# Kernel tuning notes

Measured on AMD Instinct MI355X. Metric: run time of the kernel, lower is better.

## Reference

```python
import jax, jax.numpy as jnp
import numpy as np

TWO_PI = 6.283185  # constant used verbatim in the original module


def setup_inputs() -> dict:
    key = jax.random.key(0)
    ks = jax.random.split(key, 12)
    N, input_size, light_freq, H = 8388608, 11, 16, 16
    d_in = input_size - 2 + 2 * light_freq  # 41
    x = jax.random.uniform(ks[0], (N, input_size), dtype=jnp.float32)
    B_light = jax.random.normal(ks[1], (2, light_freq), dtype=jnp.float32)
    W1 = jax.random.normal(ks[2], (d_in, H), dtype=jnp.float32) * (1.0 / np.sqrt(d_in))
    b1 = jax.random.normal(ks[3], (H,), dtype=jnp.float32) * 0.01
    W2 = jax.random.normal(ks[4], (H, H), dtype=jnp.float32) * 0.25
    b2 = jax.random.normal(ks[5], (H,), dtype=jnp.float32) * 0.01
    W3 = jax.random.normal(ks[6], (H, H), dtype=jnp.float32) * 0.25
    b3 = jax.random.normal(ks[7], (H,), dtype=jnp.float32) * 0.01
    W4 = jax.random.normal(ks[8], (H, H), dtype=jnp.float32) * 0.25
    b4 = jax.random.normal(ks[9], (H,), dtype=jnp.float32) * 0.01
    W5 = jax.random.normal(ks[10], (H, 1), dtype=jnp.float32) * 0.25
    b5 = jax.random.normal(ks[11], (1,), dtype=jnp.float32) * 0.01
    return {"x": x, "B_light": B_light, "W1": W1, "b1": b1, "W2": W2, "b2": b2,
            "W3": W3, "b3": b3, "W4": W4, "b4": b4, "W5": W5, "b5": b5}


def reference(x, B_light, W1, b1, W2, b2, W3, b3, W4, b4, W5, b5):
    # Fourier-feature encoding of the last two input dims (light direction)
    x_light = TWO_PI * (x[:, -2:] @ B_light)                      # [N, F]
    feats = jnp.concatenate([x[:, :-2], jnp.cos(x_light), jnp.sin(x_light)], axis=-1)  # [N, 41]
    # Tiny 5-layer MLP with ELU activations
    h = jax.nn.elu(feats @ W1 + b1)
    h = jax.nn.elu(h @ W2 + b2)
    h = jax.nn.elu(h @ W3 + b3)
    h = jax.nn.elu(h @ W4 + b4)
    out = h @ W5 + b5                                             # [N, 1]
    return out
```

## Files before the change

### kernel.cpp

```cpp
#include <hip/hip_runtime.h>

typedef __fp16   cvt16x2 __attribute__((ext_vector_type(2)));
typedef _Float16 h2      __attribute__((ext_vector_type(2)));
typedef _Float16 half4_t __attribute__((ext_vector_type(4)));
typedef unsigned uint2v  __attribute__((ext_vector_type(2)));
typedef float    f32x4   __attribute__((ext_vector_type(4)));

#define CH 8

#if !__has_builtin(__builtin_elementwise_exp2)
extern "C" __device__ _Float16 __ocml_exp2_f16(_Float16);
#endif

__device__ __forceinline__ unsigned pk(float a, float b) {
    cvt16x2 h = __builtin_amdgcn_cvt_pkrtz(a, b);
    return __builtin_bit_cast(unsigned, h);
}
__device__ __forceinline__ half4_t mkfrag(unsigned lo, unsigned hi) {
    uint2v u; u[0] = lo; u[1] = hi;
    return __builtin_bit_cast(half4_t, u);
}

__device__ __forceinline__ unsigned elu_pk(float a, float b) {
    h2 v = __builtin_bit_cast(h2, __builtin_amdgcn_cvt_pkrtz(a, b));
    const h2 z  = {(_Float16)0.f, (_Float16)0.f};
    const h2 lg = {(_Float16)1.44269504f, (_Float16)1.44269504f};
    const h2 m1 = {(_Float16)-1.f, (_Float16)-1.f};
    h2 t = __builtin_elementwise_min(v, z) * lg;
#if __has_builtin(__builtin_elementwise_exp2)
    h2 ev = __builtin_elementwise_exp2(t);
#else
    h2 ev; ev[0] = __ocml_exp2_f16(t[0]); ev[1] = __ocml_exp2_f16(t[1]);
#endif
    h2 r = __builtin_elementwise_max(v, ev + m1);
    return __builtin_bit_cast(unsigned, r);
}

__device__ __forceinline__ float hdot2(unsigned a, unsigned b, float c) {
#if __has_builtin(__builtin_amdgcn_fdot2)
    return __builtin_amdgcn_fdot2(__builtin_bit_cast(cvt16x2, a),
                                  __builtin_bit_cast(cvt16x2, b), c, false);
#else
    h2 av = __builtin_bit_cast(h2, a), bv = __builtin_bit_cast(h2, b);
    return fmaf((float)av[1], (float)bv[1], fmaf((float)av[0], (float)bv[0], c));
#endif
}

__global__ __launch_bounds__(128, 4) void pixenc_mfma6(
    const float* __restrict__ x,
    const float* __restrict__ Bl,
    const float* __restrict__ W1, const float* __restrict__ b1,
    const float* __restrict__ W2, const float* __restrict__ b2,
    const float* __restrict__ W3, const float* __restrict__ b3,
    const float* __restrict__ W4, const float* __restrict__ b4,
    const float* __restrict__ W5, const float* __restrict__ b5,
    float* __restrict__ out)
{
    const int t    = threadIdx.x;
    const int lane = t & 63;
    const int w    = t >> 6;
    const int g    = lane >> 4;
    const int m    = lane & 15;

    half4_t A1[3], A2, A3, A4;
    #pragma unroll
    for (int e = 0; e < 4; ++e) {
        const int c0 = 4 * e + g;
        A1[0][e] = (c0 < 9) ? (_Float16)W1[c0 * 16 + m] : (_Float16)0.f;
        A1[1][e] = (_Float16)W1[(9  + g * 4 + e) * 16 + m];
        A1[2][e] = (_Float16)W1[(25 + g * 4 + e) * 16 + m];
        A2[e]    = (_Float16)W2[(g * 4 + e) * 16 + m];
        A3[e]    = (_Float16)W3[(g * 4 + e) * 16 + m];
        A4[e]    = (_Float16)W4[(g * 4 + e) * 16 + m];
    }
    f32x4 c1, c2, c3, c4;
    float blc[4], bls[4];
    #pragma unroll
    for (int e = 0; e < 4; ++e) {
        const int r = g * 4 + e;
        c1[e] = b1[r]; c2[e] = b2[r]; c3[e] = b3[r]; c4[e] = b4[r];
        blc[e] = Bl[r]; bls[e] = Bl[16 + r];
    }
    const unsigned w5p0 = pk(W5[g * 4 + 0], W5[g * 4 + 1]);
    const unsigned w5p1 = pk(W5[g * 4 + 2], W5[g * 4 + 3]);
    const float b5v = b5[0];

    const int wavebase = blockIdx.x * (128 * CH) + w * (64 * CH);

    const float* aA = x + (size_t)(wavebase + m) * 11 + g;
    const float* aB = x + (size_t)(wavebase + m) * 11 + 8;
    float* outp = out + wavebase + lane;

    unsigned cp0[4], cp8[4];
    float cx9[4], cx10[4];
    #pragma unroll
    for (int s = 0; s < 4; ++s) {
        const float a0 = aA[s * 176], a1 = aA[s * 176 + 4];
        const float b8 = aB[s * 176], b9 = aB[s * 176 + 1], b10 = aB[s * 176 + 2];
        cp0[s] = pk(a0, a1); cp8[s] = pk(b8, 0.f);
        cx9[s] = b9; cx10[s] = b10;
    }

    #pragma unroll
    for (int c = 0; c < CH; ++c) {
        unsigned np0[4], np8[4];
        float nx9[4], nx10[4];
        if (c + 1 < CH) {
            aA += 704; aB += 704;
            #pragma unroll
            for (int s = 0; s < 4; ++s) {
                const float a0 = aA[s * 176], a1 = aA[s * 176 + 4];
                const float b8 = aB[s * 176], b9 = aB[s * 176 + 1], b10 = aB[s * 176 + 2];
                np0[s] = pk(a0, a1); np8[s] = pk(b8, 0.f);
                nx9[s] = b9; nx10[s] = b10;
            }
        }

        f32x4 acc[4];
        #pragma unroll
        for (int s = 0; s < 4; ++s) {
            float cs[4], sn[4];
            #pragma unroll
            for (int e = 0; e < 4; ++e) {
                float zz = fmaf(cx9[s], blc[e], cx10[s] * bls[e]);
                zz = __builtin_amdgcn_fractf(zz);
                cs[e] = __builtin_amdgcn_cosf(zz);
                sn[e] = __builtin_amdgcn_sinf(zz);
            }
            const half4_t F0 = mkfrag(cp0[s], cp8[s]);
            const half4_t F1 = mkfrag(pk(cs[0], cs[1]), pk(cs[2], cs[3]));
            const half4_t F2 = mkfrag(pk(sn[0], sn[1]), pk(sn[2], sn[3]));
            f32x4 a = c1;
            a = __builtin_amdgcn_mfma_f32_16x16x16f16(A1[0], F0, a, 0, 0, 0);
            a = __builtin_amdgcn_mfma_f32_16x16x16f16(A1[1], F1, a, 0, 0, 0);
            a = __builtin_amdgcn_mfma_f32_16x16x16f16(A1[2], F2, a, 0, 0, 0);
            acc[s] = a;
        }

        half4_t H[4];
        #pragma unroll
        for (int s = 0; s < 4; ++s)
            H[s] = mkfrag(elu_pk(acc[s][0], acc[s][1]), elu_pk(acc[s][2], acc[s][3]));
        #pragma unroll
        for (int s = 0; s < 4; ++s)
            acc[s] = __builtin_amdgcn_mfma_f32_16x16x16f16(A2, H[s], c2, 0, 0, 0);

        #pragma unroll
        for (int s = 0; s < 4; ++s)
            H[s] = mkfrag(elu_pk(acc[s][0], acc[s][1]), elu_pk(acc[s][2], acc[s][3]));
        #pragma unroll
        for (int s = 0; s < 4; ++s)
            acc[s] = __builtin_amdgcn_mfma_f32_16x16x16f16(A3, H[s], c3, 0, 0, 0);

        #pragma unroll
        for (int s = 0; s < 4; ++s)
            H[s] = mkfrag(elu_pk(acc[s][0], acc[s][1]), elu_pk(acc[s][2], acc[s][3]));
        #pragma unroll
        for (int s = 0; s < 4; ++s)
            acc[s] = __builtin_amdgcn_mfma_f32_16x16x16f16(A4, H[s], c4, 0, 0, 0);

        float p[4];
        #pragma unroll
        for (int s = 0; s < 4; ++s) {
            const unsigned u0 = elu_pk(acc[s][0], acc[s][1]);
            const unsigned u1 = elu_pk(acc[s][2], acc[s][3]);
            p[s] = hdot2(u1, w5p1, hdot2(u0, w5p0, 0.f));
        }
        #pragma unroll
        for (int s = 0; s < 4; ++s) p[s] += __shfl_xor(p[s], 16, 64);
        #pragma unroll
        for (int s = 0; s < 4; ++s) p[s] += __shfl_xor(p[s], 32, 64);

        const float v01 = (g & 1) ? p[1] : p[0];
        const float v23 = (g & 1) ? p[3] : p[2];
        const float v   = (g & 2) ? v23 : v01;
        outp[c * 64] = v + b5v;

        if (c + 1 < CH) {
            #pragma unroll
            for (int s = 0; s < 4; ++s) {
                cp0[s] = np0[s]; cp8[s] = np8[s];
                cx9[s] = nx9[s]; cx10[s] = nx10[s];
            }
        }
    }
}

__global__ void pixenc_tail(
    const float* __restrict__ x, const float* __restrict__ Bl,
    const float* __restrict__ W1, const float* __restrict__ b1,
    const float* __restrict__ W2, const float* __restrict__ b2,
    const float* __restrict__ W3, const float* __restrict__ b3,
    const float* __restrict__ W4, const float* __restrict__ b4,
    const float* __restrict__ W5, const float* __restrict__ b5,
    float* __restrict__ out, int N, int start)
{
    const int i = start + blockIdx.x * 256 + threadIdx.x;
    if (i >= N) return;
    const float* xr = x + (size_t)i * 11;
    float feats[41];
    for (int k = 0; k < 9; ++k) feats[k] = xr[k];
    for (int f = 0; f < 16; ++f) {
        const float ang = 6.283185f * (xr[9] * Bl[f] + xr[10] * Bl[16 + f]);
        float s, c; __sincosf(ang, &s, &c);
        feats[9 + f] = c; feats[25 + f] = s;
    }
    float h[16], gg[16];
    for (int j = 0; j < 16; ++j) h[j] = b1[j];
    for (int k = 0; k < 41; ++k)
        for (int j = 0; j < 16; ++j) h[j] = fmaf(feats[k], W1[k * 16 + j], h[j]);
    for (int j = 0; j < 16; ++j) h[j] = h[j] > 0.f ? h[j] : __expf(h[j]) - 1.f;
    for (int j = 0; j < 16; ++j) gg[j] = b2[j];
    for (int k = 0; k < 16; ++k)
        for (int j = 0; j < 16; ++j) gg[j] = fmaf(h[k], W2[k * 16 + j], gg[j]);
    for (int j = 0; j < 16; ++j) gg[j] = gg[j] > 0.f ? gg[j] : __expf(gg[j]) - 1.f;
    for (int j = 0; j < 16; ++j) h[j] = b3[j];
    for (int k = 0; k < 16; ++k)
        for (int j = 0; j < 16; ++j) h[j] = fmaf(gg[k], W3[k * 16 + j], h[j]);
    for (int j = 0; j < 16; ++j) h[j] = h[j] > 0.f ? h[j] : __expf(h[j]) - 1.f;
    for (int j = 0; j < 16; ++j) gg[j] = b4[j];
    for (int k = 0; k < 16; ++k)
        for (int j = 0; j < 16; ++j) gg[j] = fmaf(h[k], W4[k * 16 + j], gg[j]);
    for (int j = 0; j < 16; ++j) gg[j] = gg[j] > 0.f ? gg[j] : __expf(gg[j]) - 1.f;
    float o = b5[0];
    for (int j = 0; j < 16; ++j) o = fmaf(gg[j], W5[j], o);
    out[i] = o;
}

extern "C" void kernel_launch(void* const* d_in, const int* in_sizes, int n_in,
                              void* d_out, int out_size, void* d_ws, size_t ws_size,
                              hipStream_t stream) {
    const float* x  = (const float*)d_in[0];
    const float* Bl = (const float*)d_in[1];
    const float* W1 = (const float*)d_in[2];
    const float* b1 = (const float*)d_in[3];
    const float* W2 = (const float*)d_in[4];
    const float* b2 = (const float*)d_in[5];
    const float* W3 = (const float*)d_in[6];
    const float* b3 = (const float*)d_in[7];
    const float* W4 = (const float*)d_in[8];
    const float* b4 = (const float*)d_in[9];
    const float* W5 = (const float*)d_in[10];
    const float* b5 = (const float*)d_in[11];
    float* out = (float*)d_out;

    const int N = out_size;
    const int NB = N / (128 * CH);
    const int rem = N - NB * (128 * CH);
    if (NB > 0)
        pixenc_mfma6<<<NB, 128, 0, stream>>>(x, Bl, W1, b1, W2, b2, W3, b3,
                                             W4, b4, W5, b5, out);
    if (rem > 0)
        pixenc_tail<<<(rem + 255) / 256, 256, 0, stream>>>(
            x, Bl, W1, b1, W2, b2, W3, b3, W4, b4, W5, b5, out, N, NB * 128 * CH);
}
```

Baseline: 137.7 us.

## Move Fourier projection and final output layer onto MFMA instructions

Computes the light-direction projection x[9:11]·B_light with an extra fp16 MFMA per sub-tile instead of per-lane FMAs, and replaces the final 16->1 layer's fdot2 plus two cross-lane shuffles with an MFMA against a zero-padded W5 fragment, storing one result per sub-tile from the g==0 lanes. This removes VALU work and shuffle traffic in favour of the otherwise lightly used matrix unit. In exchange the projection inputs are rounded to fp16 before the fract/sin/cos, which loses phase precision, and the output stores become narrower 16-lane writes issued four times per chunk.

```diff
diff --git a/kernel.cpp b/kernel.cpp
--- a/kernel.cpp
+++ b/kernel.cpp
@@ -36,17 +36,7 @@
     return __builtin_bit_cast(unsigned, r);
 }
 
-__device__ __forceinline__ float hdot2(unsigned a, unsigned b, float c) {
-#if __has_builtin(__builtin_amdgcn_fdot2)
-    return __builtin_amdgcn_fdot2(__builtin_bit_cast(cvt16x2, a),
-                                  __builtin_bit_cast(cvt16x2, b), c, false);
-#else
-    h2 av = __builtin_bit_cast(h2, a), bv = __builtin_bit_cast(h2, b);
-    return fmaf((float)av[1], (float)bv[1], fmaf((float)av[0], (float)bv[0], c));
-#endif
-}
-
-__global__ __launch_bounds__(128, 4) void pixenc_mfma6(
+__global__ __launch_bounds__(128, 4) void pixenc_mfma7(
     const float* __restrict__ x,
     const float* __restrict__ Bl,
     const float* __restrict__ W1, const float* __restrict__ b1,
@@ -73,38 +63,39 @@
         A3[e]    = (_Float16)W3[(g * 4 + e) * 16 + m];
         A4[e]    = (_Float16)W4[(g * 4 + e) * 16 + m];
     }
+    const half4_t Az = (g == 0) ? mkfrag(pk(Bl[m], Bl[16 + m]), 0u)
+                                : mkfrag(0u, 0u);
+    const half4_t A5 = (m == 0)
+        ? mkfrag(pk(W5[g * 4 + 0], W5[g * 4 + 1]), pk(W5[g * 4 + 2], W5[g * 4 + 3]))
+        : mkfrag(0u, 0u);
     f32x4 c1, c2, c3, c4;
-    float blc[4], bls[4];
     #pragma unroll
     for (int e = 0; e < 4; ++e) {
         const int r = g * 4 + e;
         c1[e] = b1[r]; c2[e] = b2[r]; c3[e] = b3[r]; c4[e] = b4[r];
-        blc[e] = Bl[r]; bls[e] = Bl[16 + r];
-    }
-    const unsigned w5p0 = pk(W5[g * 4 + 0], W5[g * 4 + 1]);
-    const unsigned w5p1 = pk(W5[g * 4 + 2], W5[g * 4 + 3]);
+    }
     const float b5v = b5[0];
+    const unsigned zmask = (g == 0) ? 0xFFFFFFFFu : 0u;
+    const f32x4 zero4 = {0.f, 0.f, 0.f, 0.f};
 
     const int wavebase = blockIdx.x * (128 * CH) + w * (64 * CH);
 
     const float* aA = x + (size_t)(wavebase + m) * 11 + g;
     const float* aB = x + (size_t)(wavebase + m) * 11 + 8;
-    float* outp = out + wavebase + lane;
-
-    unsigned cp0[4], cp8[4];
-    float cx9[4], cx10[4];
+    float* outp = out + wavebase + m;
+
+    unsigned cp0[4], cp8[4], cbz[4];
     #pragma unroll
     for (int s = 0; s < 4; ++s) {
         const float a0 = aA[s * 176], a1 = aA[s * 176 + 4];
         const float b8 = aB[s * 176], b9 = aB[s * 176 + 1], b10 = aB[s * 176 + 2];
         cp0[s] = pk(a0, a1); cp8[s] = pk(b8, 0.f);
-        cx9[s] = b9; cx10[s] = b10;
+        cbz[s] = pk(b9, b10) & zmask;
     }
 
     #pragma unroll
     for (int c = 0; c < CH; ++c) {
-        unsigned np0[4], np8[4];
-        float nx9[4], nx10[4];
+        unsigned np0[4], np8[4], nbz[4];
         if (c + 1 < CH) {
             aA += 704; aB += 704;
             #pragma unroll
@@ -112,9 +103,15 @@
                 const float a0 = aA[s * 176], a1 = aA[s * 176 + 4];
                 const float b8 = aB[s * 176], b9 = aB[s * 176 + 1], b10 = aB[s * 176 + 2];
                 np0[s] = pk(a0, a1); np8[s] = pk(b8, 0.f);
-                nx9[s] = b9; nx10[s] = b10;
+                nbz[s] = pk(b9, b10) & zmask;
             }
         }
+
+        f32x4 az[4];
+        #pragma unroll
+        for (int s = 0; s < 4; ++s)
+            az[s] = __builtin_amdgcn_mfma_f32_16x16x16f16(
+                        Az, mkfrag(cbz[s], 0u), zero4, 0, 0, 0);
 
         f32x4 acc[4];
         #pragma unroll
@@ -122,10 +119,9 @@
             float cs[4], sn[4];
             #pragma unroll
             for (int e = 0; e < 4; ++e) {
-                float zz = fmaf(cx9[s], blc[e], cx10[s] * bls[e]);
-                zz = __builtin_amdgcn_fractf(zz);
-                cs[e] = __builtin_amdgcn_cosf(zz);
-                sn[e] = __builtin_amdgcn_sinf(zz);
+                const float zf = __builtin_amdgcn_fractf(az[s][e]);
+                cs[e] = __builtin_amdgcn_cosf(zf);
+                sn[e] = __builtin_amdgcn_sinf(zf);
             }
             const half4_t F0 = mkfrag(cp0[s], cp8[s]);
             const half4_t F1 = mkfrag(pk(cs[0], cs[1]), pk(cs[2], cs[3]));
@@ -159,28 +155,20 @@
         for (int s = 0; s < 4; ++s)
             acc[s] = __builtin_amdgcn_mfma_f32_16x16x16f16(A4, H[s], c4, 0, 0, 0);
 
-        float p[4];
+        #pragma unroll
+        for (int s = 0; s < 4; ++s)
+            H[s] = mkfrag(elu_pk(acc[s][0], acc[s][1]), elu_pk(acc[s][2], acc[s][3]));
         #pragma unroll
         for (int s = 0; s < 4; ++s) {
-            const unsigned u0 = elu_pk(acc[s][0], acc[s][1]);
-            const unsigned u1 = elu_pk(acc[s][2], acc[s][3]);
-            p[s] = hdot2(u1, w5p1, hdot2(u0, w5p0, 0.f));
-        }
-        #pragma unroll
-        for (int s = 0; s < 4; ++s) p[s] += __shfl_xor(p[s], 16, 64);
-        #pragma unroll
-        for (int s = 0; s < 4; ++s) p[s] += __shfl_xor(p[s], 32, 64);
-
-        const float v01 = (g & 1) ? p[1] : p[0];
-        const float v23 = (g & 1) ? p[3] : p[2];
-        const float v   = (g & 2) ? v23 : v01;
-        outp[c * 64] = v + b5v;
+            const f32x4 oh = __builtin_amdgcn_mfma_f32_16x16x16f16(
+                                 A5, H[s], zero4, 0, 0, 0);
+            if (g == 0) outp[c * 64 + s * 16] = oh[0] + b5v;
+        }
 
         if (c + 1 < CH) {
             #pragma unroll
             for (int s = 0; s < 4; ++s) {
-                cp0[s] = np0[s]; cp8[s] = np8[s];
-                cx9[s] = nx9[s]; cx10[s] = nx10[s];
+                cp0[s] = np0[s]; cp8[s] = np8[s]; cbz[s] = nbz[s];
             }
         }
     }
@@ -248,7 +236,7 @@
     const int NB = N / (128 * CH);
     const int rem = N - NB * (128 * CH);
     if (NB > 0)
-        pixenc_mfma6<<<NB, 128, 0, stream>>>(x, Bl, W1, b1, W2, b2, W3, b3,
+        pixenc_mfma7<<<NB, 128, 0, stream>>>(x, Bl, W1, b1, W2, b2, W3, b3,
                                              W4, b4, W5, b5, out);
     if (rem > 0)
         pixenc_tail<<<(rem + 255) / 256, 256, 0, stream>>>(
```

Result: faster. 130.8 us (-5.0%).
